# Kernel optimization log

Hardware: AMD Instinct MI355X
Metric: run time of the kernel (lower is better)

The kernel has to match this reference:

```python
import jax, jax.numpy as jnp
import numpy as np

N_NODES = 50000
N_EDGES = 1600000
IN_DIM, HID, OUT = 128, 64, 32


def _glorot(key, fan_in, fan_out):
    s = 1.0 / np.sqrt(fan_in)
    return jax.random.uniform(key, (fan_in, fan_out), jnp.float32, -s, s)


def setup_inputs() -> dict:
    key = jax.random.key(0)
    ks = jax.random.split(key, 12)
    x = jax.random.normal(ks[0], (N_NODES, IN_DIM), jnp.float32)
    edge_index = jax.random.randint(ks[1], (2, N_EDGES), 0, N_NODES, jnp.int32)
    inp = {"x": x, "edge_index": edge_index}
    # 4 SAGEConv layers: (in->hid), (hid->hid), (hid->hid), (hid->hid)
    dims = [(IN_DIM, HID), (HID, HID), (HID, HID), (HID, HID)]
    names = ["1a", "1b", "2a", "2b"]
    for i, ((di, do), nm) in enumerate(zip(dims, names)):
        k1, k2 = jax.random.split(ks[2 + i])
        inp[f"W{nm}_l"] = _glorot(k1, di, do)       # neighbor transform (with bias)
        inp[f"b{nm}"] = jnp.zeros((do,), jnp.float32)
        inp[f"W{nm}_r"] = _glorot(k2, di, do)       # root/self transform (no bias)
    inp["Wlin"] = _glorot(ks[10], HID, OUT)
    inp["blin"] = jnp.zeros((OUT,), jnp.float32)
    return inp


def _sage(h, src, dst, Wl, bl, Wr, n_nodes):
    # SAGEConv: out = mean_{j in N(i)} x_j @ Wl + bl + x_i @ Wr
    msg = h[src]                                                    # [E, D] gather
    ssum = jax.ops.segment_sum(msg, dst, num_segments=n_nodes)     # [N, D] scatter-add
    cnt = jax.ops.segment_sum(jnp.ones((src.shape[0], 1), h.dtype), dst, num_segments=n_nodes)
    agg = ssum / jnp.maximum(cnt, 1.0)                              # mean; 0 for isolated nodes
    return agg @ Wl + bl + h @ Wr


def reference(x, edge_index, W1a_l, b1a, W1a_r, W1b_l, b1b, W1b_r,
              W2a_l, b2a, W2a_r, W2b_l, b2b, W2b_r, Wlin, blin):
    src, dst = edge_index[0], edge_index[1]
    n = x.shape[0]
    # conv1 = GraphSAGE(2 layers): sage -> relu -> sage ; then outer F.relu
    h = jax.nn.relu(_sage(x, src, dst, W1a_l, b1a, W1a_r, n))
    h = jax.nn.relu(_sage(h, src, dst, W1b_l, b1b, W1b_r, n))
    # conv2 = GraphSAGE(2 layers): sage -> relu -> sage (no final act)
    h = jax.nn.relu(_sage(h, src, dst, W2a_l, b2a, W2a_r, n))
    h = _sage(h, src, dst, W2b_l, b2b, W2b_r, n)
    return h @ Wlin + blin
```

## Files before the change

kernel.cpp:

```cpp
#include <hip/hip_runtime.h>
#include <hip/hip_fp16.h>


#define CHUNK 4096
#define SLICE_W 512
#define MAXS 128

__global__ __launch_bounds__(256) void hist_pack(
    const int* __restrict__ e32, unsigned* __restrict__ pe,
    int* __restrict__ counts, int E, int S, int Bpad)
{
    __shared__ int h[MAXS];
    const int tid = threadIdx.x, b = blockIdx.x;
    for (int i = tid; i < S; i += 256) h[i] = 0;
    __syncthreads();
    const int lo = b * CHUNK, hi = min(lo + CHUNK, E);
    for (int e = lo + tid; e < hi; e += 256) {
        const int s = e32[e];
        const int d = e32[E + e];
        pe[e] = ((unsigned)s << 16) | (unsigned)d;
        atomicAdd(&h[d >> 9], 1);
    }
    __syncthreads();
    for (int i = tid; i < S; i += 256) counts[i * Bpad + b] = h[i];
}

__global__ __launch_bounds__(512) void scan_cols(
    int* __restrict__ counts, int* __restrict__ stotal, int B, int Bpad)
{
    __shared__ int sc[512];
    const int s = blockIdx.x, tid = threadIdx.x;
    const int v = (tid < B) ? counts[s * Bpad + tid] : 0;
    sc[tid] = v;
    __syncthreads();
    for (int off = 1; off < 512; off <<= 1) {
        const int a = (tid >= off) ? sc[tid - off] : 0;
        __syncthreads();
        sc[tid] += a;
        __syncthreads();
    }
    if (tid < B) counts[s * Bpad + tid] = sc[tid] - v;
    if (tid == 0) stotal[s] = sc[511];
}

__global__ __launch_bounds__(MAXS) void scan_slices(
    const int* __restrict__ stotal, int* __restrict__ sbase, int S)
{
    __shared__ int sc[MAXS];
    const int tid = threadIdx.x;
    const int v = (tid < S) ? stotal[tid] : 0;
    sc[tid] = v;
    __syncthreads();
    for (int off = 1; off < MAXS; off <<= 1) {
        const int a = (tid >= off) ? sc[tid - off] : 0;
        __syncthreads();
        sc[tid] += a;
        __syncthreads();
    }
    if (tid < S) sbase[tid] = sc[tid] - v;
}

__global__ __launch_bounds__(256) void bucket_scatter(
    const unsigned* __restrict__ pe, const int* __restrict__ counts,
    const int* __restrict__ sbase, unsigned* __restrict__ bedge,
    int E, int S, int Bpad)
{
    __shared__ int h[MAXS];
    const int tid = threadIdx.x, b = blockIdx.x;
    for (int i = tid; i < S; i += 256) h[i] = 0;
    __syncthreads();
    const int lo = b * CHUNK, hi = min(lo + CHUNK, E);
    for (int e = lo + tid; e < hi; e += 256) {
        const unsigned v = pe[e];
        const int sl = (int)(v & 0xFFFFu) >> 9;
        const int r = atomicAdd(&h[sl], 1);
        bedge[sbase[sl] + counts[sl * Bpad + b] + r] = v;
    }
}

__global__ __launch_bounds__(1024) void csr_fill(
    const unsigned* __restrict__ bedge, const int* __restrict__ stotal,
    const int* __restrict__ sbase, int* __restrict__ row_ptr,
    float* __restrict__ inv, unsigned short* __restrict__ adj, int N, int E)
{
    __shared__ int cnt[SLICE_W];
    __shared__ int sc[SLICE_W];
    const int s = blockIdx.x, tid = threadIdx.x;
    const int n = stotal[s], base = sbase[s];
    if (tid < SLICE_W) cnt[tid] = 0;
    __syncthreads();
    for (int i = tid; i < n; i += 1024)
        atomicAdd(&cnt[bedge[base + i] & (SLICE_W - 1)], 1);
    __syncthreads();
    if (tid < SLICE_W) sc[tid] = cnt[tid];
    __syncthreads();
    for (int off = 1; off < SLICE_W; off <<= 1) {
        int a = 0;
        if (tid < SLICE_W && tid >= off) a = sc[tid - off];
        __syncthreads();
        if (tid < SLICE_W) sc[tid] += a;
        __syncthreads();
    }
    if (tid < SLICE_W) {
        const int c = cnt[tid];
        const int excl = sc[tid] - c;
        const int node = (s << 9) + tid;
        if (node < N) {
            row_ptr[node] = base + excl;
            inv[node] = 1.0f / (float)(c > 0 ? c : 1);
        }
        cnt[tid] = excl;
    }
    __syncthreads();
    for (int i = tid; i < n; i += 1024) {
        const unsigned v = bedge[base + i];
        const int p = atomicAdd(&cnt[v & (SLICE_W - 1)], 1);
        adj[base + p] = (unsigned short)(v >> 16);
    }
    if (s == 0 && tid == 0) row_ptr[N] = E;
}

template<bool RELU>
__global__ __launch_bounds__(256) void gather_fused(
    const __half* __restrict__ t, const unsigned short* __restrict__ adj,
    const int* __restrict__ row_ptr, const float* __restrict__ inv,
    const __half* __restrict__ u, float* __restrict__ out, int N)
{
    const int node = (blockIdx.x * 256 + threadIdx.x) >> 6;
    const int lane = threadIdx.x & 63;
    const int grp  = lane >> 3;
    const int d0   = (lane & 7) * 8;
    if (node >= N) return;
    const int beg = row_ptr[node], end = row_ptr[node + 1];
    float a[8] = {0.f, 0.f, 0.f, 0.f, 0.f, 0.f, 0.f, 0.f};
    int j = beg + grp;
    for (; j + 8 < end; j += 16) {
        const int n0 = adj[j], n1 = adj[j + 8];
        const float4 p0 = *(const float4*)(t + (size_t)n0 * 64 + d0);
        const float4 p1 = *(const float4*)(t + (size_t)n1 * 64 + d0);
        const __half2* h0 = (const __half2*)&p0;
        const __half2* h1 = (const __half2*)&p1;
        #pragma unroll
        for (int k = 0; k < 4; ++k) {
            float2 f0 = __half22float2(h0[k]);
            float2 f1 = __half22float2(h1[k]);
            a[2 * k]     += f0.x + f1.x;
            a[2 * k + 1] += f0.y + f1.y;
        }
    }
    if (j < end) {
        const float4 p0 = *(const float4*)(t + (size_t)adj[j] * 64 + d0);
        const __half2* h0 = (const __half2*)&p0;
        #pragma unroll
        for (int k = 0; k < 4; ++k) {
            float2 f0 = __half22float2(h0[k]);
            a[2 * k]     += f0.x;
            a[2 * k + 1] += f0.y;
        }
    }
    #pragma unroll
    for (int k = 0; k < 8; ++k) {
        a[k] += __shfl_xor(a[k], 8);
        a[k] += __shfl_xor(a[k], 16);
        a[k] += __shfl_xor(a[k], 32);
    }
    if (grp == 0) {
        const float vi = inv[node];
        const float4 uv = *(const float4*)(u + (size_t)node * 64 + d0);
        const __half2* uh = (const __half2*)&uv;
        float4 o0, o1;
        {
            float2 g0 = __half22float2(uh[0]);
            float2 g1 = __half22float2(uh[1]);
            float2 g2 = __half22float2(uh[2]);
            float2 g3 = __half22float2(uh[3]);
            o0.x = g0.x + a[0] * vi; o0.y = g0.y + a[1] * vi;
            o0.z = g1.x + a[2] * vi; o0.w = g1.y + a[3] * vi;
            o1.x = g2.x + a[4] * vi; o1.y = g2.y + a[5] * vi;
            o1.z = g3.x + a[6] * vi; o1.w = g3.y + a[7] * vi;
        }
        if (RELU) {
            o0.x = fmaxf(o0.x, 0.f); o0.y = fmaxf(o0.y, 0.f);
            o0.z = fmaxf(o0.z, 0.f); o0.w = fmaxf(o0.w, 0.f);
            o1.x = fmaxf(o1.x, 0.f); o1.y = fmaxf(o1.y, 0.f);
            o1.z = fmaxf(o1.z, 0.f); o1.w = fmaxf(o1.w, 0.f);
        }
        *(float4*)(out + (size_t)node * 64 + d0)     = o0;
        *(float4*)(out + (size_t)node * 64 + d0 + 4) = o1;
    }
}

template<int K>
__global__ __launch_bounds__(256) void mm_dual(
    const float* __restrict__ A, const float* __restrict__ Wl,
    const float* __restrict__ Wr, const float* __restrict__ bias,
    __half* __restrict__ T, __half* __restrict__ U, int M)
{
    __shared__ float As[64][68];
    __shared__ float Wls[64 * 64];
    __shared__ float Wrs[64 * 64];
    const int tid  = threadIdx.x;
    const int row0 = blockIdx.x * 64;
    const int tx = tid & 15, ty = tid >> 4;
    float accT[4][4] = {{0.f}}, accU[4][4] = {{0.f}};

    for (int kc = 0; kc < K; kc += 64) {
        for (int i = tid * 4; i < 64 * 64; i += 1024) {
            int r = i >> 6, c = i & 63;
            int gr = row0 + r;
            float4 v = make_float4(0.f, 0.f, 0.f, 0.f);
            if (gr < M) v = *(const float4*)&A[(size_t)gr * K + kc + c];
            *(float4*)&As[r][c] = v;
        }
        for (int i = tid * 4; i < 64 * 64; i += 1024) {
            *(float4*)&Wls[i] = *(const float4*)&Wl[kc * 64 + i];
            *(float4*)&Wrs[i] = *(const float4*)&Wr[kc * 64 + i];
        }
        __syncthreads();
        #pragma unroll 4
        for (int kk = 0; kk < 64; ++kk) {
            float a[4];
            #pragma unroll
            for (int r = 0; r < 4; ++r) a[r] = As[ty * 4 + r][kk];
            float bl[4], br[4];
            #pragma unroll
            for (int c = 0; c < 4; ++c) {
                bl[c] = Wls[kk * 64 + tx * 4 + c];
                br[c] = Wrs[kk * 64 + tx * 4 + c];
            }
            #pragma unroll
            for (int r = 0; r < 4; ++r)
                #pragma unroll
                for (int c = 0; c < 4; ++c) {
                    accT[r][c] += a[r] * bl[c];
                    accU[r][c] += a[r] * br[c];
                }
        }
        __syncthreads();
    }

    const float4 bv = *(const float4*)&bias[tx * 4];
    #pragma unroll
    for (int r = 0; r < 4; ++r) {
        int gr = row0 + ty * 4 + r;
        if (gr >= M) continue;
        union { int2 v; __half2 h[2]; } tp;
        tp.h[0] = __floats2half2_rn(accT[r][0], accT[r][1]);
        tp.h[1] = __floats2half2_rn(accT[r][2], accT[r][3]);
        *(int2*)&T[(size_t)gr * 64 + tx * 4] = tp.v;
        union { int2 v; __half2 h[2]; } up;
        up.h[0] = __floats2half2_rn(accU[r][0] + bv.x, accU[r][1] + bv.y);
        up.h[1] = __floats2half2_rn(accU[r][2] + bv.z, accU[r][3] + bv.w);
        *(int2*)&U[(size_t)gr * 64 + tx * 4] = up.v;
    }
}

__global__ __launch_bounds__(256) void mm_lin(
    const float* __restrict__ A, const float* __restrict__ W,
    const float* __restrict__ bias, float* __restrict__ C, int M)
{
    __shared__ float As[64][68];
    __shared__ float Ws[64 * 32];
    const int tid  = threadIdx.x;
    const int row0 = blockIdx.x * 64;

    for (int i = tid * 4; i < 64 * 32; i += 1024) {
        *(float4*)&Ws[i] = *(const float4*)&W[i];
    }
    for (int i = tid * 4; i < 64 * 64; i += 1024) {
        int r = i >> 6, c = i & 63;
        int gr = row0 + r;
        float4 v = make_float4(0.f, 0.f, 0.f, 0.f);
        if (gr < M) v = *(const float4*)&A[(size_t)gr * 64 + c];
        *(float4*)&As[r][c] = v;
    }
    __syncthreads();

    const int tx = tid & 15, ty = tid >> 4;
    float acc[4][2] = {{0.f}};
    #pragma unroll 4
    for (int kk = 0; kk < 64; ++kk) {
        float a[4];
        #pragma unroll
        for (int r = 0; r < 4; ++r) a[r] = As[ty * 4 + r][kk];
        float b0 = Ws[kk * 32 + tx * 2];
        float b1 = Ws[kk * 32 + tx * 2 + 1];
        #pragma unroll
        for (int r = 0; r < 4; ++r) {
            acc[r][0] += a[r] * b0;
            acc[r][1] += a[r] * b1;
        }
    }
    #pragma unroll
    for (int r = 0; r < 4; ++r) {
        int gr = row0 + ty * 4 + r;
        if (gr >= M) continue;
        float2 o = make_float2(acc[r][0] + bias[tx * 2],
                               acc[r][1] + bias[tx * 2 + 1]);
        *(float2*)&C[(size_t)gr * 32 + tx * 2] = o;
    }
}

extern "C" void kernel_launch(void* const* d_in, const int* in_sizes, int n_in,
                              void* d_out, int out_size, void* d_ws, size_t ws_size,
                              hipStream_t stream) {
    const float* x     = (const float*)d_in[0];
    const int*   ei    = (const int*)  d_in[1];
    const float* W1a_l = (const float*)d_in[2];
    const float* b1a   = (const float*)d_in[3];
    const float* W1a_r = (const float*)d_in[4];
    const float* W1b_l = (const float*)d_in[5];
    const float* b1b   = (const float*)d_in[6];
    const float* W1b_r = (const float*)d_in[7];
    const float* W2a_l = (const float*)d_in[8];
    const float* b2a   = (const float*)d_in[9];
    const float* W2a_r = (const float*)d_in[10];
    const float* W2b_l = (const float*)d_in[11];
    const float* b2b   = (const float*)d_in[12];
    const float* W2b_r = (const float*)d_in[13];
    const float* Wlin  = (const float*)d_in[14];
    const float* blin  = (const float*)d_in[15];

    const int N = in_sizes[0] / 128;
    const int E = in_sizes[1] / 2;
    const int S = (N + SLICE_W - 1) / SLICE_W;
    const int B = (E + CHUNK - 1) / CHUNK;
    const int Bpad = (B + 15) & ~15;

    size_t o = 0;
    auto take = [&](size_t bytes) -> void* {
        void* p = (char*)d_ws + o;
        o += (bytes + 255) & ~(size_t)255;
        return p;
    };
    unsigned*       pe      = (unsigned*)take((size_t)E * 4);
    unsigned*       bedge   = (unsigned*)take((size_t)E * 4);
    int*            counts  = (int*)   take((size_t)S * Bpad * 4);
    int*            stotal  = (int*)   take((size_t)S * 4);
    int*            sbase   = (int*)   take((size_t)S * 4);
    int*            row_ptr = (int*)   take((size_t)(N + 1) * 4);
    float*          inv     = (float*) take((size_t)N * 4);
    unsigned short* adj     = (unsigned short*)take((size_t)E * 2);
    __half*         t       = (__half*)take((size_t)N * 64 * 2);
    __half*         u       = (__half*)take((size_t)N * 64 * 2);
    float*          hA      = (float*) take((size_t)N * 64 * 4);
    float*          hB      = (float*) take((size_t)N * 64 * 4);
    (void)ws_size; (void)n_in; (void)out_size;

    const int mb = (N + 63) / 64;
    const int gb = (N * 64 + 255) / 256;

    hist_pack<<<B, 256, 0, stream>>>(ei, pe, counts, E, S, Bpad);
    scan_cols<<<S, 512, 0, stream>>>(counts, stotal, B, Bpad);
    scan_slices<<<1, MAXS, 0, stream>>>(stotal, sbase, S);
    bucket_scatter<<<B, 256, 0, stream>>>(pe, counts, sbase, bedge, E, S, Bpad);
    csr_fill<<<S, 1024, 0, stream>>>(bedge, stotal, sbase, row_ptr, inv, adj, N, E);

    mm_dual<128><<<mb, 256, 0, stream>>>(x, W1a_l, W1a_r, b1a, t, u, N);
    gather_fused<true><<<gb, 256, 0, stream>>>(t, adj, row_ptr, inv, u, hA, N);
    mm_dual<64><<<mb, 256, 0, stream>>>(hA, W1b_l, W1b_r, b1b, t, u, N);
    gather_fused<true><<<gb, 256, 0, stream>>>(t, adj, row_ptr, inv, u, hB, N);
    mm_dual<64><<<mb, 256, 0, stream>>>(hB, W2a_l, W2a_r, b2a, t, u, N);
    gather_fused<true><<<gb, 256, 0, stream>>>(t, adj, row_ptr, inv, u, hA, N);
    mm_dual<64><<<mb, 256, 0, stream>>>(hA, W2b_l, W2b_r, b2b, t, u, N);
    gather_fused<false><<<gb, 256, 0, stream>>>(t, adj, row_ptr, inv, u, hB, N);
    mm_lin<<<mb, 256, 0, stream>>>(hB, Wlin, blin, (float*)d_out, N);
}
```

Before: 270.1 us.

## Fuse final linear into last gather and read A directly in mm_dual

The last SAGE gather now also applies the 64x32 output linear layer in registers, using cross-lane shuffles. This removes the mm_lin kernel and the write and re-read of the final hidden buffer. mm_dual no longer stages A rows in shared memory; each thread loads its own A rows as float4 straight from global memory, which saves LDS traffic and a barrier but sends redundant global loads through the cache. The two hidden buffers are merged into one, and the template ReLU switch is dropped.

```diff
diff --git a/kernel.cpp b/kernel.cpp
--- a/kernel.cpp
+++ b/kernel.cpp
@@ -120,7 +120,6 @@
     if (s == 0 && tid == 0) row_ptr[N] = E;
 }
 
-template<bool RELU>
 __global__ __launch_bounds__(256) void gather_fused(
     const __half* __restrict__ t, const unsigned short* __restrict__ adj,
     const int* __restrict__ row_ptr, const float* __restrict__ inv,
@@ -179,14 +178,93 @@
             o1.x = g2.x + a[4] * vi; o1.y = g2.y + a[5] * vi;
             o1.z = g3.x + a[6] * vi; o1.w = g3.y + a[7] * vi;
         }
-        if (RELU) {
-            o0.x = fmaxf(o0.x, 0.f); o0.y = fmaxf(o0.y, 0.f);
-            o0.z = fmaxf(o0.z, 0.f); o0.w = fmaxf(o0.w, 0.f);
-            o1.x = fmaxf(o1.x, 0.f); o1.y = fmaxf(o1.y, 0.f);
-            o1.z = fmaxf(o1.z, 0.f); o1.w = fmaxf(o1.w, 0.f);
-        }
+        o0.x = fmaxf(o0.x, 0.f); o0.y = fmaxf(o0.y, 0.f);
+        o0.z = fmaxf(o0.z, 0.f); o0.w = fmaxf(o0.w, 0.f);
+        o1.x = fmaxf(o1.x, 0.f); o1.y = fmaxf(o1.y, 0.f);
+        o1.z = fmaxf(o1.z, 0.f); o1.w = fmaxf(o1.w, 0.f);
         *(float4*)(out + (size_t)node * 64 + d0)     = o0;
         *(float4*)(out + (size_t)node * 64 + d0 + 4) = o1;
+    }
+}
+
+__global__ __launch_bounds__(256) void gather_lin(
+    const __half* __restrict__ t, const unsigned short* __restrict__ adj,
+    const int* __restrict__ row_ptr, const float* __restrict__ inv,
+    const __half* __restrict__ u, const float* __restrict__ Wlin,
+    const float* __restrict__ blin, float* __restrict__ out, int N)
+{
+    const int node = (blockIdx.x * 256 + threadIdx.x) >> 6;
+    const int lane = threadIdx.x & 63;
+    const int grp  = lane >> 3;
+    const int d0   = (lane & 7) * 8;
+    if (node >= N) return;
+    float4 w[8];
+    #pragma unroll
+    for (int k = 0; k < 8; ++k)
+        w[k] = *(const float4*)&Wlin[(d0 + k) * 32 + 4 * grp];
+
+    const int beg = row_ptr[node], end = row_ptr[node + 1];
+    float a[8] = {0.f, 0.f, 0.f, 0.f, 0.f, 0.f, 0.f, 0.f};
+    int j = beg + grp;
+    for (; j + 8 < end; j += 16) {
+        const int n0 = adj[j], n1 = adj[j + 8];
+        const float4 p0 = *(const float4*)(t + (size_t)n0 * 64 + d0);
+        const float4 p1 = *(const float4*)(t + (size_t)n1 * 64 + d0);
+        const __half2* h0 = (const __half2*)&p0;
+        const __half2* h1 = (const __half2*)&p1;
+        #pragma unroll
+        for (int k = 0; k < 4; ++k) {
+            float2 f0 = __half22float2(h0[k]);
+            float2 f1 = __half22float2(h1[k]);
+            a[2 * k]     += f0.x + f1.x;
+            a[2 * k + 1] += f0.y + f1.y;
+        }
+    }
+    if (j < end) {
+        const float4 p0 = *(const float4*)(t + (size_t)adj[j] * 64 + d0);
+        const __half2* h0 = (const __half2*)&p0;
+        #pragma unroll
+        for (int k = 0; k < 4; ++k) {
+            float2 f0 = __half22float2(h0[k]);
+            a[2 * k]     += f0.x;
+            a[2 * k + 1] += f0.y;
+        }
+    }
+    #pragma unroll
+    for (int k = 0; k < 8; ++k) {
+        a[k] += __shfl_xor(a[k], 8);
+        a[k] += __shfl_xor(a[k], 16);
+        a[k] += __shfl_xor(a[k], 32);
+    }
+    const float vi = inv[node];
+    const float4 uv = *(const float4*)(u + (size_t)node * 64 + d0);
+    const __half2* uh = (const __half2*)&uv;
+    float h[8];
+    {
+        float2 g0 = __half22float2(uh[0]);
+        float2 g1 = __half22float2(uh[1]);
+        float2 g2 = __half22float2(uh[2]);
+        float2 g3 = __half22float2(uh[3]);
+        h[0] = g0.x + a[0] * vi; h[1] = g0.y + a[1] * vi;
+        h[2] = g1.x + a[2] * vi; h[3] = g1.y + a[3] * vi;
+        h[4] = g2.x + a[4] * vi; h[5] = g2.y + a[5] * vi;
+        h[6] = g3.x + a[6] * vi; h[7] = g3.y + a[7] * vi;
+    }
+    float p0 = 0.f, p1 = 0.f, p2 = 0.f, p3 = 0.f;
+    #pragma unroll
+    for (int k = 0; k < 8; ++k) {
+        p0 += h[k] * w[k].x; p1 += h[k] * w[k].y;
+        p2 += h[k] * w[k].z; p3 += h[k] * w[k].w;
+    }
+    #pragma unroll
+    for (int m = 1; m < 8; m <<= 1) {
+        p0 += __shfl_xor(p0, m); p1 += __shfl_xor(p1, m);
+        p2 += __shfl_xor(p2, m); p3 += __shfl_xor(p3, m);
+    }
+    if ((lane & 7) == 0) {
+        const float4 bv = *(const float4*)&blin[4 * grp];
+        float4 o = make_float4(p0 + bv.x, p1 + bv.y, p2 + bv.z, p3 + bv.w);
+        *(float4*)&out[(size_t)node * 32 + 4 * grp] = o;
     }
 }
 
@@ -196,7 +274,6 @@
     const float* __restrict__ Wr, const float* __restrict__ bias,
     __half* __restrict__ T, __half* __restrict__ U, int M)
 {
-    __shared__ float As[64][68];
     __shared__ float Wls[64 * 64];
     __shared__ float Wrs[64 * 64];
     const int tid  = threadIdx.x;
@@ -204,46 +281,55 @@
     const int tx = tid & 15, ty = tid >> 4;
     float accT[4][4] = {{0.f}}, accU[4][4] = {{0.f}};
 
+    const float* Arow[4];
+    bool val[4];
+    #pragma unroll
+    for (int r = 0; r < 4; ++r) {
+        const int gr = row0 + ty * 4 + r;
+        val[r] = (gr < M);
+        Arow[r] = A + (size_t)(val[r] ? gr : 0) * K;
+    }
+
     for (int kc = 0; kc < K; kc += 64) {
-        for (int i = tid * 4; i < 64 * 64; i += 1024) {
-            int r = i >> 6, c = i & 63;
-            int gr = row0 + r;
-            float4 v = make_float4(0.f, 0.f, 0.f, 0.f);
-            if (gr < M) v = *(const float4*)&A[(size_t)gr * K + kc + c];
-            *(float4*)&As[r][c] = v;
-        }
+        if (kc) __syncthreads();
         for (int i = tid * 4; i < 64 * 64; i += 1024) {
             *(float4*)&Wls[i] = *(const float4*)&Wl[kc * 64 + i];
             *(float4*)&Wrs[i] = *(const float4*)&Wr[kc * 64 + i];
         }
         __syncthreads();
-        #pragma unroll 4
-        for (int kk = 0; kk < 64; ++kk) {
-            float a[4];
-            #pragma unroll
-            for (int r = 0; r < 4; ++r) a[r] = As[ty * 4 + r][kk];
-            float bl[4], br[4];
-            #pragma unroll
-            for (int c = 0; c < 4; ++c) {
-                bl[c] = Wls[kk * 64 + tx * 4 + c];
-                br[c] = Wrs[kk * 64 + tx * 4 + c];
-            }
+        for (int kk4 = 0; kk4 < 16; ++kk4) {
+            float4 a4[4];
             #pragma unroll
             for (int r = 0; r < 4; ++r)
+                a4[r] = val[r] ? *(const float4*)&Arow[r][kc + kk4 * 4]
+                               : make_float4(0.f, 0.f, 0.f, 0.f);
+            #pragma unroll
+            for (int q = 0; q < 4; ++q) {
+                const int kk = kk4 * 4 + q;
+                float bl[4], br[4];
                 #pragma unroll
                 for (int c = 0; c < 4; ++c) {
-                    accT[r][c] += a[r] * bl[c];
-                    accU[r][c] += a[r] * br[c];
+                    bl[c] = Wls[kk * 64 + tx * 4 + c];
+                    br[c] = Wrs[kk * 64 + tx * 4 + c];
                 }
-        }
-        __syncthreads();
+                #pragma unroll
+                for (int r = 0; r < 4; ++r) {
+                    const float av = ((const float*)&a4[r])[q];
+                    #pragma unroll
+                    for (int c = 0; c < 4; ++c) {
+                        accT[r][c] += av * bl[c];
+                        accU[r][c] += av * br[c];
+                    }
+                }
+            }
+        }
     }
 
     const float4 bv = *(const float4*)&bias[tx * 4];
     #pragma unroll
     for (int r = 0; r < 4; ++r) {
-        int gr = row0 + ty * 4 + r;
-        if (gr >= M) continue;
+        if (!val[r]) continue;
+        const int gr = row0 + ty * 4 + r;
         union { int2 v; __half2 h[2]; } tp;
         tp.h[0] = __floats2half2_rn(accT[r][0], accT[r][1]);
         tp.h[1] = __floats2half2_rn(accT[r][2], accT[r][3]);
@@ -252,52 +338,6 @@
         up.h[0] = __floats2half2_rn(accU[r][0] + bv.x, accU[r][1] + bv.y);
         up.h[1] = __floats2half2_rn(accU[r][2] + bv.z, accU[r][3] + bv.w);
         *(int2*)&U[(size_t)gr * 64 + tx * 4] = up.v;
-    }
-}
-
-__global__ __launch_bounds__(256) void mm_lin(
-    const float* __restrict__ A, const float* __restrict__ W,
-    const float* __restrict__ bias, float* __restrict__ C, int M)
-{
-    __shared__ float As[64][68];
-    __shared__ float Ws[64 * 32];
-    const int tid  = threadIdx.x;
-    const int row0 = blockIdx.x * 64;
-
-    for (int i = tid * 4; i < 64 * 32; i += 1024) {
-        *(float4*)&Ws[i] = *(const float4*)&W[i];
-    }
-    for (int i = tid * 4; i < 64 * 64; i += 1024) {
-        int r = i >> 6, c = i & 63;
-        int gr = row0 + r;
-        float4 v = make_float4(0.f, 0.f, 0.f, 0.f);
-        if (gr < M) v = *(const float4*)&A[(size_t)gr * 64 + c];
-        *(float4*)&As[r][c] = v;
-    }
-    __syncthreads();
-
-    const int tx = tid & 15, ty = tid >> 4;
-    float acc[4][2] = {{0.f}};
-    #pragma unroll 4
-    for (int kk = 0; kk < 64; ++kk) {
-        float a[4];
-        #pragma unroll
-        for (int r = 0; r < 4; ++r) a[r] = As[ty * 4 + r][kk];
-        float b0 = Ws[kk * 32 + tx * 2];
-        float b1 = Ws[kk * 32 + tx * 2 + 1];
-        #pragma unroll
-        for (int r = 0; r < 4; ++r) {
-            acc[r][0] += a[r] * b0;
-            acc[r][1] += a[r] * b1;
-        }
-    }
-    #pragma unroll
-    for (int r = 0; r < 4; ++r) {
-        int gr = row0 + ty * 4 + r;
-        if (gr >= M) continue;
-        float2 o = make_float2(acc[r][0] + bias[tx * 2],
-                               acc[r][1] + bias[tx * 2 + 1]);
-        *(float2*)&C[(size_t)gr * 32 + tx * 2] = o;
     }
 }
 
@@ -343,8 +383,7 @@
     unsigned short* adj     = (unsigned short*)take((size_t)E * 2);
     __half*         t       = (__half*)take((size_t)N * 64 * 2);
     __half*         u       = (__half*)take((size_t)N * 64 * 2);
-    float*          hA      = (float*) take((size_t)N * 64 * 4);
-    float*          hB      = (float*) take((size_t)N * 64 * 4);
+    float*          h       = (float*) take((size_t)N * 64 * 4);
     (void)ws_size; (void)n_in; (void)out_size;
 
     const int mb = (N + 63) / 64;
@@ -357,12 +396,12 @@
     csr_fill<<<S, 1024, 0, stream>>>(bedge, stotal, sbase, row_ptr, inv, adj, N, E);
 
     mm_dual<128><<<mb, 256, 0, stream>>>(x, W1a_l, W1a_r, b1a, t, u, N);
-    gather_fused<true><<<gb, 256, 0, stream>>>(t, adj, row_ptr, inv, u, hA, N);
-    mm_dual<64><<<mb, 256, 0, stream>>>(hA, W1b_l, W1b_r, b1b, t, u, N);
-    gather_fused<true><<<gb, 256, 0, stream>>>(t, adj, row_ptr, inv, u, hB, N);
-    mm_dual<64><<<mb, 256, 0, stream>>>(hB, W2a_l, W2a_r, b2a, t, u, N);
-    gather_fused<true><<<gb, 256, 0, stream>>>(t, adj, row_ptr, inv, u, hA, N);
-    mm_dual<64><<<mb, 256, 0, stream>>>(hA, W2b_l, W2b_r, b2b, t, u, N);
-    gather_fused<false><<<gb, 256, 0, stream>>>(t, adj, row_ptr, inv, u, hB, N);
-    mm_lin<<<mb, 256, 0, stream>>>(hB, Wlin, blin, (float*)d_out, N);
-}
+    gather_fused<<<gb, 256, 0, stream>>>(t, adj, row_ptr, inv, u, h, N);
+    mm_dual<64><<<mb, 256, 0, stream>>>(h, W1b_l, W1b_r, b1b, t, u, N);
+    gather_fused<<<gb, 256, 0, stream>>>(t, adj, row_ptr, inv, u, h, N);
+    mm_dual<64><<<mb, 256, 0, stream>>>(h, W2a_l, W2a_r, b2a, t, u, N);
+    gather_fused<<<gb, 256, 0, stream>>>(t, adj, row_ptr, inv, u, h, N);
+    mm_dual<64><<<mb, 256, 0, stream>>>(h, W2b_l, W2b_r, b2b, t, u, N);
+    gather_lin<<<gb, 256, 0, stream>>>(t, adj, row_ptr, inv, u, Wlin, blin,
+                                       (float*)d_out, N);
+}
```

Result: slower. 323.6 us (+19.8%).
